# Performance work log

Measured on AMD Instinct MI355X. Metric: run time of the kernel, lower is better.

## Reference

```python
import jax, jax.numpy as jnp
import numpy as np

EPS = 1e-5

def _ln(x, g, b):
    mu = jnp.mean(x, axis=-1, keepdims=True)
    var = jnp.mean(jnp.square(x - mu), axis=-1, keepdims=True)
    return (x - mu) * jax.lax.rsqrt(var + EPS) * g + b

def setup_inputs() -> dict:
    B, T, D, E, H, M = 2, 2048, 1024, 8, 512, 2048
    key = jax.random.key(0)
    ks = jax.random.split(key, 24)
    s = 0.02
    inp = {}
    inp['x'] = jax.random.normal(ks[0], (B, T, D), jnp.float32)
    flat = jnp.arange(M, dtype=jnp.int32) * 2  # unique token ids over B*T
    inp['index_b'] = flat // T
    inp['index_t'] = flat % T
    # shared SwiGLU (hidden = H)
    inp['sw1'] = jax.random.normal(ks[1], (H, D), jnp.float32) * s
    inp['sb1'] = jnp.zeros((H,), jnp.float32)
    inp['sw2'] = jax.random.normal(ks[2], (H, D), jnp.float32) * s
    inp['sb2'] = jnp.zeros((H,), jnp.float32)
    inp['sw3'] = jax.random.normal(ks[3], (D, H), jnp.float32) * s
    inp['sb3'] = jnp.zeros((D,), jnp.float32)
    inp['s_ln_g'] = jnp.ones((H,), jnp.float32)
    inp['s_ln_b'] = jnp.zeros((H,), jnp.float32)
    # gates
    inp['sg_w'] = jax.random.normal(ks[4], (1, D), jnp.float32) * s
    inp['sg_b'] = jnp.zeros((1,), jnp.float32)
    inp['eg_w'] = jax.random.normal(ks[5], (E, D), jnp.float32) * s
    inp['eg_b'] = jnp.zeros((E,), jnp.float32)
    inp['exp_bias'] = jnp.zeros((E,), jnp.float32)
    # per-expert SwiGLU stacks
    inp['ew1'] = jax.random.normal(ks[6], (E, H, D), jnp.float32) * s
    inp['eb1'] = jnp.zeros((E, H), jnp.float32)
    inp['ew2'] = jax.random.normal(ks[7], (E, H, D), jnp.float32) * s
    inp['eb2'] = jnp.zeros((E, H), jnp.float32)
    inp['ew3'] = jax.random.normal(ks[8], (E, D, H), jnp.float32) * s
    inp['eb3'] = jnp.zeros((E, D), jnp.float32)
    inp['sel_ln_g'] = jnp.ones((H,), jnp.float32)
    inp['sel_ln_b'] = jnp.zeros((H,), jnp.float32)
    return inp

def _forward(x, index_b, index_t, sw1, sb1, sw2, sb2, sw3, sb3, s_ln_g, s_ln_b,
             sg_w, sg_b, eg_w, eg_b, exp_bias, ew1, eb1, ew2, eb2, ew3, eb3,
             sel_ln_g, sel_ln_b):
    # shared SwiGLU over all tokens: [B,T,D]
    x1 = jnp.einsum('btd,hd->bth', x, sw1) + sb1
    x2 = jnp.einsum('btd,hd->bth', x, sw2) + sb2
    sh = _ln(jax.nn.silu(x1) * x2, s_ln_g, s_ln_b)
    shared_out = jnp.einsum('bth,dh->btd', sh, sw3) + sb3
    # MoE tokens
    x_moe = x[index_b, index_t]  # [M,D]
    shared_scores = jax.nn.sigmoid(x_moe @ sg_w.T + sg_b)       # [M,1]
    expert_scores = jax.nn.sigmoid(x_moe @ eg_w.T + eg_b)       # [M,E]
    top1_idx = jnp.argmax(expert_scores + exp_bias, axis=-1)    # [M]
    top1_score = jnp.take_along_axis(expert_scores, top1_idx[:, None], axis=-1)  # [M,1]
    weights = jax.nn.softmax(jnp.concatenate([shared_scores, top1_score], axis=-1), axis=-1)
    shared_w, expert_w = weights[:, 0], weights[:, 1]
    shared_moe_out = shared_out[index_b, index_t] * shared_w[:, None]
    # per-expert SwiGLU computed densely for all E, then token selects its expert
    h1 = jnp.einsum('md,ehd->meh', x_moe, ew1) + eb1  # [M,E,H]
    h2 = jnp.einsum('md,ehd->meh', x_moe, ew2) + eb2
    z = _ln(jax.nn.silu(h1) * h2, sel_ln_g, sel_ln_b)
    out_all = jnp.einsum('meh,edh->med', z, ew3) + eb3  # [M,E,D]
    expert_out = jnp.take_along_axis(out_all, top1_idx[:, None, None], axis=1)[:, 0]  # [M,D]
    expert_moe_out = expert_out * expert_w[:, None]
    final_out = shared_out.at[index_b, index_t].set(shared_moe_out + expert_moe_out)
    return final_out

def reference(x, index_b, index_t, sw1, sb1, sw2, sb2, sw3, sb3, s_ln_g, s_ln_b,
              sg_w, sg_b, eg_w, eg_b, exp_bias, ew1, eb1, ew2, eb2, ew3, eb3,
              sel_ln_g, sel_ln_b):
    return _forward(x, index_b, index_t, sw1, sb1, sw2, sb2, sw3, sb3, s_ln_g, s_ln_b,
                    sg_w, sg_b, eg_w, eg_b, exp_bias, ew1, eb1, ew2, eb2, ew3, eb3,
                    sel_ln_g, sel_ln_b)
```

## Files before the change

### kernel.cpp

```cpp
#include <hip/hip_runtime.h>
#include <cstdint>

typedef unsigned short u16;
typedef __bf16 bf16x8 __attribute__((ext_vector_type(8)));
typedef float f32x4 __attribute__((ext_vector_type(4)));

#define T_SEQ  2048
#define D_DIM  1024
#define H_DIM  512
#define E_NUM  8
#define M_TOK  2048
#define BT_TOK 4096
#define MAXP   3072

static __device__ __forceinline__ u16 f2bf(float f) {
    union { float f; uint32_t u; } v; v.f = f;
    uint32_t u = v.u;
    return (u16)((u + 0x7FFFu + ((u >> 16) & 1u)) >> 16);
}
static __device__ __forceinline__ uint32_t pack2(float a, float b) {
    return (uint32_t)f2bf(a) | ((uint32_t)f2bf(b) << 16);
}

static __device__ __forceinline__ void gl_lds16(const u16* g, u16* l) {
    __builtin_amdgcn_global_load_lds(
        (const __attribute__((address_space(1))) uint32_t*)g,
        (__attribute__((address_space(3))) uint32_t*)l, 16, 0, 0);
}

__global__ __launch_bounds__(256)
void cvt_all_kernel(const float* __restrict__ x,
                    const float* __restrict__ sw1, const float* __restrict__ sw2,
                    const float* __restrict__ sw3,
                    const float* __restrict__ ew1, const float* __restrict__ ew2,
                    const float* __restrict__ ew3,
                    u16* __restrict__ xb,
                    u16* __restrict__ sw1b, u16* __restrict__ sw2b, u16* __restrict__ sw3b,
                    u16* __restrict__ ew1b, u16* __restrict__ ew2b, u16* __restrict__ ew3b)
{
    long i = (long)blockIdx.x * 256 + threadIdx.x;
    const float* s; u16* d; long off;
    if      (i < 1048576) { s = x;   d = xb;   off = i; }
    else if (i < 1179648) { s = sw1; d = sw1b; off = i - 1048576; }
    else if (i < 1310720) { s = sw2; d = sw2b; off = i - 1179648; }
    else if (i < 1441792) { s = sw3; d = sw3b; off = i - 1310720; }
    else if (i < 2490368) { s = ew1; d = ew1b; off = i - 1441792; }
    else if (i < 3538944) { s = ew2; d = ew2b; off = i - 2490368; }
    else                  { s = ew3; d = ew3b; off = i - 3538944; }
    float4 v = ((const float4*)s)[off];
    uint2 o;
    o.x = pack2(v.x, v.y);
    o.y = pack2(v.z, v.w);
    ((uint2*)d)[off] = o;
}

__global__ __launch_bounds__(256)
void gating_kernel(const float* __restrict__ x,
                   const int* __restrict__ ib, const int* __restrict__ itx,
                   const float* __restrict__ sgw, const float* __restrict__ sgb,
                   const float* __restrict__ egw, const float* __restrict__ egb,
                   const float* __restrict__ ebias,
                   float* __restrict__ shw, float* __restrict__ expw,
                   int* __restrict__ top1, int* __restrict__ rowidx)
{
    int m = blockIdx.x, tid = threadIdx.x;
    __shared__ float xs[D_DIM];
    __shared__ float sc[9];
    int row = ib[m] * T_SEQ + itx[m];
    if (tid == 0) rowidx[m] = row;
    const float* xr = x + (size_t)row * D_DIM;
    ((float4*)xs)[tid] = ((const float4*)xr)[tid];
    __syncthreads();
    int lane = tid & 63, w = tid >> 6;
    for (int sidx = w; sidx < 9; sidx += 4) {
        const float* wr = (sidx == 0) ? sgw : (egw + (size_t)(sidx - 1) * D_DIM);
        float acc = 0.f;
        for (int i = lane; i < D_DIM; i += 64) acc += xs[i] * wr[i];
        #pragma unroll
        for (int o = 32; o > 0; o >>= 1) acc += __shfl_xor(acc, o);
        if (lane == 0) sc[sidx] = acc;
    }
    __syncthreads();
    if (tid == 0) {
        float ss = 1.f / (1.f + expf(-(sc[0] + sgb[0])));
        float es[E_NUM];
        float best = -1e30f; int bi = 0;
        #pragma unroll
        for (int e = 0; e < E_NUM; ++e) {
            es[e] = 1.f / (1.f + expf(-(sc[1 + e] + egb[e])));
            float t = es[e] + ebias[e];
            if (t > best) { best = t; bi = e; }
        }
        float ts = es[bi];
        shw[m]  = 1.f / (1.f + expf(ts - ss));
        expw[m] = 1.f / (1.f + expf(ss - ts));
        top1[m] = bi;
    }
}

__global__ void bucket_kernel(const int* __restrict__ top1,
                              int* __restrict__ base, int* __restrict__ cnt,
                              int* __restrict__ perm)
{
    __shared__ int lc[E_NUM], lb[E_NUM + 1], cur[E_NUM];
    int tid = threadIdx.x;
    if (tid < E_NUM) { lc[tid] = 0; cur[tid] = 0; }
    __syncthreads();
    for (int m = tid; m < M_TOK; m += 256) atomicAdd(&lc[top1[m]], 1);
    __syncthreads();
    if (tid == 0) {
        int bacc = 0;
        for (int e = 0; e < E_NUM; ++e) { lb[e] = bacc; bacc += (lc[e] + 63) & ~63; }
        lb[E_NUM] = bacc;
    }
    __syncthreads();
    for (int m = tid; m < M_TOK; m += 256) {
        int e = top1[m];
        int pos = lb[e] + atomicAdd(&cur[e], 1);
        perm[pos] = m;
    }
    if (tid <= E_NUM) base[tid] = lb[tid];
    if (tid < E_NUM)  cnt[tid]  = lc[tid];
}

template<bool SEL>
__global__ __launch_bounds__(256)
void ln_kernel(const float* __restrict__ X,
               const float* __restrict__ g, const float* __restrict__ b,
               u16* __restrict__ out,
               const int* __restrict__ base, const int* __restrict__ cnt)
{
    int m = blockIdx.x;
    int tid = threadIdx.x;
    if (SEL) {
        bool valid = false;
        int tot = base[E_NUM];
        if (m < tot) {
            int e = 0;
            while (!(m >= base[e] && m < base[e + 1])) ++e;
            valid = (m - base[e]) < cnt[e];
        }
        if (!valid) {
            out[(size_t)m * H_DIM + tid] = 0;
            out[(size_t)m * H_DIM + tid + 256] = 0;
            return;
        }
    }
    const float* row = X + (size_t)m * D_DIM;
    float a0 = row[tid],       c0 = row[H_DIM + tid];
    float a1 = row[tid + 256], c1 = row[H_DIM + tid + 256];
    float v0 = (a0 / (1.f + expf(-a0))) * c0;
    float v1 = (a1 / (1.f + expf(-a1))) * c1;
    float s = v0 + v1, s2 = v0 * v0 + v1 * v1;
    #pragma unroll
    for (int o = 32; o > 0; o >>= 1) {
        s  += __shfl_xor(s, o);
        s2 += __shfl_xor(s2, o);
    }
    __shared__ float red[8];
    int w = tid >> 6;
    if ((tid & 63) == 0) { red[w] = s; red[4 + w] = s2; }
    __syncthreads();
    s  = red[0] + red[1] + red[2] + red[3];
    s2 = red[4] + red[5] + red[6] + red[7];
    float mu  = s * (1.f / H_DIM);
    float var = s2 * (1.f / H_DIM) - mu * mu;
    float inv = rsqrtf(var + 1e-5f);
    out[(size_t)m * H_DIM + tid]       = f2bf((v0 - mu) * inv * g[tid] + b[tid]);
    out[(size_t)m * H_DIM + tid + 256] = f2bf((v1 - mu) * inv * g[tid + 256] + b[tid + 256]);
}

template<int MODE, int KLEN>
__global__ __launch_bounds__(256, 4)
void gemm_kernel(const u16* __restrict__ A, int lda,
                 const u16* __restrict__ W0, const u16* __restrict__ W1, int nsplit,
                 const float* __restrict__ b0, const float* __restrict__ b1,
                 float* __restrict__ C,
                 const int* __restrict__ base, const int* __restrict__ cnt,
                 const int* __restrict__ perm, const int* __restrict__ rowidx,
                 const float* __restrict__ shw, const float* __restrict__ expw)
{
    constexpr int NITER = KLEN / 64;
    const int tid   = threadIdx.x;
    const int bn    = blockIdx.x;
    const int bm    = blockIdx.y;
    const int mbase = bm * 64;

    int pend = 0;
    if (MODE >= 2) {
        const int tot = base[E_NUM];
        if (mbase >= tot) return;
        int e = 0;
        while (!(mbase >= base[e] && mbase < base[e + 1])) ++e;
        pend = base[e] + cnt[e];
        if (mbase >= pend) return;
        const size_t wstride = (size_t)H_DIM * D_DIM;
        W0 += (size_t)e * wstride;
        if (MODE == 2) W1 += (size_t)e * wstride;
        b0 += e * ((MODE == 2) ? H_DIM : D_DIM);
        if (MODE == 2) b1 += e * H_DIM;
    }

    __shared__ __align__(16) u16 lds[(64 + 128) * 64];

    const int w  = tid >> 6;
    const int l  = tid & 63;
    const int sr = tid >> 3;
    const int sc = tid & 7;

    const u16* agp[2];
    #pragma unroll
    for (int t = 0; t < 2; ++t) {
        int r = t * 32 + sr;
        int grow;
        if (MODE == 2) {
            int p  = mbase + r;
            int pp = (p < pend) ? p : (pend - 1);
            grow = rowidx[perm[pp]];
        } else {
            grow = mbase + r;
        }
        agp[t] = A + (size_t)grow * lda + (sc ^ (r & 7)) * 8;
    }
    const u16* bgp[4];
    #pragma unroll
    for (int t = 0; t < 4; ++t) {
        int r = t * 32 + sr;
        int n = bn * 128 + r;
        bgp[t] = ((n < nsplit) ? (W0 + (size_t)n * KLEN)
                               : (W1 + (size_t)(n - nsplit) * KLEN)) + (sc ^ (r & 7)) * 8;
    }

    const int l16 = l & 15, quad = l >> 4;
    const int wm = w >> 1, wn = w & 1;

    int avo[2][2], bvo[4][2];
    #pragma unroll
    for (int i = 0; i < 2; ++i) {
        int R = wm * 32 + i * 16 + l16;
        #pragma unroll
        for (int kx = 0; kx < 2; ++kx)
            avo[i][kx] = R * 128 + (((kx * 4 + quad) ^ (R & 7)) * 16);
    }
    #pragma unroll
    for (int j = 0; j < 4; ++j) {
        int R = wn * 64 + j * 16 + l16;
        #pragma unroll
        for (int kx = 0; kx < 2; ++kx)
            bvo[j][kx] = 8192 + R * 128 + (((kx * 4 + quad) ^ (R & 7)) * 16);
    }

    f32x4 acc[2][4];
    #pragma unroll
    for (int i = 0; i < 2; ++i)
        #pragma unroll
        for (int j = 0; j < 4; ++j)
            acc[i][j] = (f32x4){0.f, 0.f, 0.f, 0.f};

    const int kstart = (bm + bn * 3) & (NITER - 1);
    const char* ldsc = (const char*)lds;

    for (int it = 0; it < NITER; ++it) {
        int k0 = ((it + kstart) & (NITER - 1)) * 64;
        #pragma unroll
        for (int t = 0; t < 2; ++t)
            gl_lds16(agp[t] + k0, lds + t * 2048 + w * 512);
        #pragma unroll
        for (int t = 0; t < 4; ++t)
            gl_lds16(bgp[t] + k0, lds + 4096 + t * 2048 + w * 512);
        __syncthreads();
        #pragma unroll
        for (int kx = 0; kx < 2; ++kx) {
            bf16x8 av[2], bv[4];
            #pragma unroll
            for (int i = 0; i < 2; ++i)
                av[i] = *(const bf16x8*)(ldsc + avo[i][kx]);
            #pragma unroll
            for (int j = 0; j < 4; ++j)
                bv[j] = *(const bf16x8*)(ldsc + bvo[j][kx]);
            #pragma unroll
            for (int i = 0; i < 2; ++i)
                #pragma unroll
                for (int j = 0; j < 4; ++j)
                    acc[i][j] = __builtin_amdgcn_mfma_f32_16x16x32_bf16(av[i], bv[j], acc[i][j], 0, 0, 0);
        }
        __syncthreads();
    }

    if (MODE == 3) {
        #pragma unroll
        for (int i = 0; i < 2; ++i) {
            #pragma unroll
            for (int rr = 0; rr < 4; ++rr) {
                int p = mbase + wm * 32 + i * 16 + quad * 4 + rr;
                if (p < pend) {
                    int tok = perm[p];
                    int row = rowidx[tok];
                    float sw = shw[tok], ew = expw[tok];
                    float* outr = C + (size_t)row * D_DIM;
                    #pragma unroll
                    for (int j = 0; j < 4; ++j) {
                        int gn = bn * 128 + wn * 64 + j * 16 + l16;
                        outr[gn] = outr[gn] * sw + (acc[i][j][rr] + b0[gn]) * ew;
                    }
                }
            }
        }
    } else {
        #pragma unroll
        for (int i = 0; i < 2; ++i) {
            #pragma unroll
            for (int rr = 0; rr < 4; ++rr) {
                int gm = mbase + wm * 32 + i * 16 + quad * 4 + rr;
                float* outr = C + (size_t)gm * D_DIM;
                #pragma unroll
                for (int j = 0; j < 4; ++j) {
                    int gn = bn * 128 + wn * 64 + j * 16 + l16;
                    float bias = (gn < nsplit) ? b0[gn] : b1[gn - nsplit];
                    outr[gn] = acc[i][j][rr] + bias;
                }
            }
        }
    }
}

extern "C" void kernel_launch(void* const* d_in, const int* in_sizes, int n_in,
                              void* d_out, int out_size, void* d_ws, size_t ws_size,
                              hipStream_t stream) {
    const float* x        = (const float*)d_in[0];
    const int*   index_b  = (const int*)d_in[1];
    const int*   index_t  = (const int*)d_in[2];
    const float* sw1      = (const float*)d_in[3];
    const float* sb1      = (const float*)d_in[4];
    const float* sw2      = (const float*)d_in[5];
    const float* sb2      = (const float*)d_in[6];
    const float* sw3      = (const float*)d_in[7];
    const float* sb3      = (const float*)d_in[8];
    const float* s_ln_g   = (const float*)d_in[9];
    const float* s_ln_b   = (const float*)d_in[10];
    const float* sg_w     = (const float*)d_in[11];
    const float* sg_b     = (const float*)d_in[12];
    const float* eg_w     = (const float*)d_in[13];
    const float* eg_b     = (const float*)d_in[14];
    const float* exp_bias = (const float*)d_in[15];
    const float* ew1      = (const float*)d_in[16];
    const float* eb1      = (const float*)d_in[17];
    const float* ew2      = (const float*)d_in[18];
    const float* eb2      = (const float*)d_in[19];
    const float* ew3      = (const float*)d_in[20];
    const float* eb3      = (const float*)d_in[21];
    const float* sel_ln_g = (const float*)d_in[22];
    const float* sel_ln_b = (const float*)d_in[23];
    float* out = (float*)d_out;
    char*  ws  = (char*)d_ws;

    u16*   xb   = (u16*)(ws + 0);
    u16*   sw1b = (u16*)(ws + 8388608);
    u16*   sw2b = (u16*)(ws + 9437184);
    u16*   sw3b = (u16*)(ws + 10485760);
    u16*   ew1b = (u16*)(ws + 11534336);
    u16*   ew2b = (u16*)(ws + 19922944);
    u16*   ew3b = (u16*)(ws + 28311552);
    float* x12  = (float*)(ws + 36700160);
    float* h12  = x12;
    u16*   sh   = (u16*)(ws + 53477376);
    u16*   z    = sh;
    float* shw    = (float*)(ws + 57671680);
    float* expw   = shw + M_TOK;
    int*   top1   = (int*)(expw + M_TOK);
    int*   rowidx = top1 + M_TOK;
    int*   perm   = rowidx + M_TOK;
    int*   basep  = perm + MAXP;
    int*   cntp   = basep + 16;

    const int NSPLIT_NONE = 1 << 28;

    cvt_all_kernel<<<dim3(17920), dim3(256), 0, stream>>>(
        x, sw1, sw2, sw3, ew1, ew2, ew3,
        xb, sw1b, sw2b, sw3b, ew1b, ew2b, ew3b);

    gating_kernel<<<dim3(M_TOK), dim3(256), 0, stream>>>(x, index_b, index_t,
        sg_w, sg_b, eg_w, eg_b, exp_bias, shw, expw, top1, rowidx);
    bucket_kernel<<<dim3(1), dim3(256), 0, stream>>>(top1, basep, cntp, perm);

    gemm_kernel<0, 1024><<<dim3(8, 64), dim3(256), 0, stream>>>(
        xb, D_DIM, sw1b, sw2b, H_DIM, sb1, sb2, x12,
        basep, cntp, perm, rowidx, shw, expw);
    ln_kernel<false><<<dim3(BT_TOK), dim3(256), 0, stream>>>(
        x12, s_ln_g, s_ln_b, sh, basep, cntp);
    gemm_kernel<1, 512><<<dim3(8, 64), dim3(256), 0, stream>>>(
        sh, H_DIM, sw3b, sw3b, NSPLIT_NONE, sb3, sb3, out,
        basep, cntp, perm, rowidx, shw, expw);
    gemm_kernel<2, 1024><<<dim3(8, MAXP / 64), dim3(256), 0, stream>>>(
        xb, D_DIM, ew1b, ew2b, H_DIM, eb1, eb2, h12,
        basep, cntp, perm, rowidx, shw, expw);
    ln_kernel<true><<<dim3(MAXP), dim3(256), 0, stream>>>(
        h12, sel_ln_g, sel_ln_b, z, basep, cntp);
    gemm_kernel<3, 512><<<dim3(8, MAXP / 64), dim3(256), 0, stream>>>(
        z, H_DIM, ew3b, ew3b, NSPLIT_NONE, eb3, eb3, out,
        basep, cntp, perm, rowidx, shw, expw);
}
```

Before: 250.1 us.

## Merge independent stages into combined launches to cut kernel count

Independent stages are packed into shared grids through block-index dispatch: shared GEMM1 runs with gating, shared LN with bucketing, and shared GEMM2 with expert GEMM1. Kernel launches drop from eight to five, and independent work can fill the GPU together instead of running back to back. In exchange, the merged kernels take on the launch bounds and LDS footprint of the heaviest branch, so the light gating blocks now run with GEMM-sized shared memory and register limits.

```diff
diff --git a/kernel.cpp b/kernel.cpp
--- a/kernel.cpp
+++ b/kernel.cpp
@@ -12,6 +12,7 @@
 #define M_TOK  2048
 #define BT_TOK 4096
 #define MAXP   3072
+#define NSPLIT_NONE (1 << 28)
 
 static __device__ __forceinline__ u16 f2bf(float f) {
     union { float f; uint32_t u; } v; v.f = f;
@@ -54,18 +55,19 @@
     ((uint2*)d)[off] = o;
 }
 
-__global__ __launch_bounds__(256)
-void gating_kernel(const float* __restrict__ x,
-                   const int* __restrict__ ib, const int* __restrict__ itx,
-                   const float* __restrict__ sgw, const float* __restrict__ sgb,
-                   const float* __restrict__ egw, const float* __restrict__ egb,
-                   const float* __restrict__ ebias,
-                   float* __restrict__ shw, float* __restrict__ expw,
-                   int* __restrict__ top1, int* __restrict__ rowidx)
-{
-    int m = blockIdx.x, tid = threadIdx.x;
-    __shared__ float xs[D_DIM];
-    __shared__ float sc[9];
+
+__device__ __forceinline__ void gating_body(
+    int m,
+    const float* __restrict__ x,
+    const int* __restrict__ ib, const int* __restrict__ itx,
+    const float* __restrict__ sgw, const float* __restrict__ sgb,
+    const float* __restrict__ egw, const float* __restrict__ egb,
+    const float* __restrict__ ebias,
+    float* __restrict__ shw, float* __restrict__ expw,
+    int* __restrict__ top1, int* __restrict__ rowidx,
+    float* xs, float* sc)
+{
+    int tid = threadIdx.x;
     int row = ib[m] * T_SEQ + itx[m];
     if (tid == 0) rowidx[m] = row;
     const float* xr = x + (size_t)row * D_DIM;
@@ -98,11 +100,14 @@
     }
 }
 
-__global__ void bucket_kernel(const int* __restrict__ top1,
-                              int* __restrict__ base, int* __restrict__ cnt,
-                              int* __restrict__ perm)
-{
-    __shared__ int lc[E_NUM], lb[E_NUM + 1], cur[E_NUM];
+__device__ __forceinline__ void bucket_body(
+    const int* __restrict__ top1,
+    int* __restrict__ base, int* __restrict__ cnt, int* __restrict__ perm,
+    int* sm)
+{
+    int* lc  = sm;
+    int* lb  = sm + E_NUM;
+    int* cur = sm + 2 * E_NUM + 1;
     int tid = threadIdx.x;
     if (tid < E_NUM) { lc[tid] = 0; cur[tid] = 0; }
     __syncthreads();
@@ -124,13 +129,14 @@
 }
 
 template<bool SEL>
-__global__ __launch_bounds__(256)
-void ln_kernel(const float* __restrict__ X,
-               const float* __restrict__ g, const float* __restrict__ b,
-               u16* __restrict__ out,
-               const int* __restrict__ base, const int* __restrict__ cnt)
-{
-    int m = blockIdx.x;
+__device__ __forceinline__ void ln_body(
+    int m,
+    const float* __restrict__ X,
+    const float* __restrict__ g, const float* __restrict__ b,
+    u16* __restrict__ out,
+    const int* __restrict__ base, const int* __restrict__ cnt,
+    float* red)
+{
     int tid = threadIdx.x;
     if (SEL) {
         bool valid = false;
@@ -157,7 +163,6 @@
         s  += __shfl_xor(s, o);
         s2 += __shfl_xor(s2, o);
     }
-    __shared__ float red[8];
     int w = tid >> 6;
     if ((tid & 63) == 0) { red[w] = s; red[4 + w] = s2; }
     __syncthreads();
@@ -171,19 +176,19 @@
 }
 
 template<int MODE, int KLEN>
-__global__ __launch_bounds__(256, 4)
-void gemm_kernel(const u16* __restrict__ A, int lda,
-                 const u16* __restrict__ W0, const u16* __restrict__ W1, int nsplit,
-                 const float* __restrict__ b0, const float* __restrict__ b1,
-                 float* __restrict__ C,
-                 const int* __restrict__ base, const int* __restrict__ cnt,
-                 const int* __restrict__ perm, const int* __restrict__ rowidx,
-                 const float* __restrict__ shw, const float* __restrict__ expw)
+__device__ __forceinline__ void gemm_body(
+    int bn, int bm,
+    const u16* __restrict__ A, int lda,
+    const u16* __restrict__ W0, const u16* __restrict__ W1, int nsplit,
+    const float* __restrict__ b0, const float* __restrict__ b1,
+    float* __restrict__ C,
+    const int* __restrict__ base, const int* __restrict__ cnt,
+    const int* __restrict__ perm, const int* __restrict__ rowidx,
+    const float* __restrict__ shw, const float* __restrict__ expw,
+    u16* lds)
 {
     constexpr int NITER = KLEN / 64;
     const int tid   = threadIdx.x;
-    const int bn    = blockIdx.x;
-    const int bm    = blockIdx.y;
     const int mbase = bm * 64;
 
     int pend = 0;
@@ -200,8 +205,6 @@
         b0 += e * ((MODE == 2) ? H_DIM : D_DIM);
         if (MODE == 2) b1 += e * H_DIM;
     }
-
-    __shared__ __align__(16) u16 lds[(64 + 128) * 64];
 
     const int w  = tid >> 6;
     const int l  = tid & 63;
@@ -322,6 +325,91 @@
             }
         }
     }
+}
+
+
+__global__ __launch_bounds__(256, 4)
+void k_g1_gating(const u16* __restrict__ xb,
+                 const u16* __restrict__ sw1b, const u16* __restrict__ sw2b,
+                 const float* __restrict__ sb1, const float* __restrict__ sb2,
+                 float* __restrict__ x12,
+                 const float* __restrict__ x,
+                 const int* __restrict__ ib, const int* __restrict__ itx,
+                 const float* __restrict__ sgw, const float* __restrict__ sgb,
+                 const float* __restrict__ egw, const float* __restrict__ egb,
+                 const float* __restrict__ ebias,
+                 float* __restrict__ shw, float* __restrict__ expw,
+                 int* __restrict__ top1, int* __restrict__ rowidx)
+{
+    __shared__ __align__(16) u16 lds[(64 + 128) * 64];
+    int bx = blockIdx.x;
+    if (bx < 512) {
+        gemm_body<0, 1024>(bx & 7, bx >> 3, xb, D_DIM, sw1b, sw2b, H_DIM, sb1, sb2, x12,
+                           nullptr, nullptr, nullptr, nullptr, nullptr, nullptr, lds);
+    } else {
+        float* xs = (float*)lds;
+        float* sc = xs + D_DIM;
+        gating_body(bx - 512, x, ib, itx, sgw, sgb, egw, egb, ebias,
+                    shw, expw, top1, rowidx, xs, sc);
+    }
+}
+
+__global__ __launch_bounds__(256)
+void k_ln_bucket(const float* __restrict__ x12,
+                 const float* __restrict__ g, const float* __restrict__ b,
+                 u16* __restrict__ shn,
+                 const int* __restrict__ top1,
+                 int* __restrict__ basep, int* __restrict__ cntp, int* __restrict__ perm)
+{
+    __shared__ __align__(16) float smf[32];
+    int bx = blockIdx.x;
+    if (bx < BT_TOK) ln_body<false>(bx, x12, g, b, shn, nullptr, nullptr, smf);
+    else             bucket_body(top1, basep, cntp, perm, (int*)smf);
+}
+
+__global__ __launch_bounds__(256, 4)
+void k_g2_e1(const u16* __restrict__ shn, const u16* __restrict__ sw3b,
+             const float* __restrict__ sb3, float* __restrict__ out,
+             const u16* __restrict__ xb,
+             const u16* __restrict__ ew1b, const u16* __restrict__ ew2b,
+             const float* __restrict__ eb1, const float* __restrict__ eb2,
+             float* __restrict__ h12,
+             const int* __restrict__ basep, const int* __restrict__ cntp,
+             const int* __restrict__ perm, const int* __restrict__ rowidx)
+{
+    __shared__ __align__(16) u16 lds[(64 + 128) * 64];
+    int bx = blockIdx.x;
+    if (bx < 512) {
+        gemm_body<1, 512>(bx & 7, bx >> 3, shn, H_DIM, sw3b, sw3b, NSPLIT_NONE, sb3, sb3, out,
+                          nullptr, nullptr, nullptr, nullptr, nullptr, nullptr, lds);
+    } else {
+        int b2 = bx - 512;
+        gemm_body<2, 1024>(b2 & 7, b2 >> 3, xb, D_DIM, ew1b, ew2b, H_DIM, eb1, eb2, h12,
+                           basep, cntp, perm, rowidx, nullptr, nullptr, lds);
+    }
+}
+
+__global__ __launch_bounds__(256)
+void k_ln_sel(const float* __restrict__ h12,
+              const float* __restrict__ g, const float* __restrict__ b,
+              u16* __restrict__ z,
+              const int* __restrict__ basep, const int* __restrict__ cntp)
+{
+    __shared__ __align__(16) float smf[8];
+    ln_body<true>(blockIdx.x, h12, g, b, z, basep, cntp, smf);
+}
+
+__global__ __launch_bounds__(256, 4)
+void k_e2(const u16* __restrict__ z, const u16* __restrict__ ew3b,
+          const float* __restrict__ eb3, float* __restrict__ out,
+          const int* __restrict__ basep, const int* __restrict__ cntp,
+          const int* __restrict__ perm, const int* __restrict__ rowidx,
+          const float* __restrict__ shw, const float* __restrict__ expw)
+{
+    __shared__ __align__(16) u16 lds[(64 + 128) * 64];
+    int bx = blockIdx.x;
+    gemm_body<3, 512>(bx & 7, bx >> 3, z, H_DIM, ew3b, ew3b, NSPLIT_NONE, eb3, eb3, out,
+                      basep, cntp, perm, rowidx, shw, expw, lds);
 }
 
 extern "C" void kernel_launch(void* const* d_in, const int* in_sizes, int n_in,
@@ -373,30 +461,26 @@
     int*   basep  = perm + MAXP;
     int*   cntp   = basep + 16;
 
-    const int NSPLIT_NONE = 1 << 28;
-
     cvt_all_kernel<<<dim3(17920), dim3(256), 0, stream>>>(
         x, sw1, sw2, sw3, ew1, ew2, ew3,
         xb, sw1b, sw2b, sw3b, ew1b, ew2b, ew3b);
 
-    gating_kernel<<<dim3(M_TOK), dim3(256), 0, stream>>>(x, index_b, index_t,
-        sg_w, sg_b, eg_w, eg_b, exp_bias, shw, expw, top1, rowidx);
-    bucket_kernel<<<dim3(1), dim3(256), 0, stream>>>(top1, basep, cntp, perm);
-
-    gemm_kernel<0, 1024><<<dim3(8, 64), dim3(256), 0, stream>>>(
-        xb, D_DIM, sw1b, sw2b, H_DIM, sb1, sb2, x12,
-        basep, cntp, perm, rowidx, shw, expw);
-    ln_kernel<false><<<dim3(BT_TOK), dim3(256), 0, stream>>>(
-        x12, s_ln_g, s_ln_b, sh, basep, cntp);
-    gemm_kernel<1, 512><<<dim3(8, 64), dim3(256), 0, stream>>>(
-        sh, H_DIM, sw3b, sw3b, NSPLIT_NONE, sb3, sb3, out,
-        basep, cntp, perm, rowidx, shw, expw);
-    gemm_kernel<2, 1024><<<dim3(8, MAXP / 64), dim3(256), 0, stream>>>(
-        xb, D_DIM, ew1b, ew2b, H_DIM, eb1, eb2, h12,
-        basep, cntp, perm, rowidx, shw, expw);
-    ln_kernel<true><<<dim3(MAXP), dim3(256), 0, stream>>>(
+    k_g1_gating<<<dim3(512 + M_TOK), dim3(256), 0, stream>>>(
+        xb, sw1b, sw2b, sb1, sb2, x12,
+        x, index_b, index_t, sg_w, sg_b, eg_w, eg_b, exp_bias,
+        shw, expw, top1, rowidx);
+
+    k_ln_bucket<<<dim3(BT_TOK + 1), dim3(256), 0, stream>>>(
+        x12, s_ln_g, s_ln_b, sh, top1, basep, cntp, perm);
+
+    k_g2_e1<<<dim3(512 + 8 * (MAXP / 64)), dim3(256), 0, stream>>>(
+        sh, sw3b, sb3, out,
+        xb, ew1b, ew2b, eb1, eb2, h12,
+        basep, cntp, perm, rowidx);
+
+    k_ln_sel<<<dim3(MAXP), dim3(256), 0, stream>>>(
         h12, sel_ln_g, sel_ln_b, z, basep, cntp);
-    gemm_kernel<3, 512><<<dim3(8, MAXP / 64), dim3(256), 0, stream>>>(
-        z, H_DIM, ew3b, ew3b, NSPLIT_NONE, eb3, eb3, out,
-        basep, cntp, perm, rowidx, shw, expw);
-}
+
+    k_e2<<<dim3(8 * (MAXP / 64)), dim3(256), 0, stream>>>(
+        z, ew3b, eb3, out, basep, cntp, perm, rowidx, shw, expw);
+}
```

New measurement: 236.8 us. 1.06x faster.
